# Performance work log

Measured on AMD Instinct MI355X. Metric: run time of the kernel, lower is better.

The kernel has to match this reference:

```python
import jax, jax.numpy as jnp
import numpy as np

N_EMB = 1024
HEAD_SIZE = 64
BLOCK_SIZE = 2048
B, T = 8, 2048


def setup_inputs() -> dict:
    key = jax.random.key(0)
    kx, kq, kk, kv = jax.random.split(key, 4)
    scale = 1.0 / (N_EMB ** 0.5)
    x = jax.random.normal(kx, (B, T, N_EMB), dtype=jnp.float32)
    Wq = jax.random.uniform(kq, (N_EMB, HEAD_SIZE), dtype=jnp.float32) * scale
    Wk = jax.random.uniform(kk, (N_EMB, HEAD_SIZE), dtype=jnp.float32) * scale
    Wv = jax.random.uniform(kv, (N_EMB, HEAD_SIZE), dtype=jnp.float32) * scale
    return {"x": x, "Wq": Wq, "Wk": Wk, "Wv": Wv}


def reference(x, Wq, Wk, Wv):
    # Faithful to Head.__call__ with is_training=False.
    # NOTE: original code applies NO 1/sqrt(head_size) scaling to the scores.
    Bt, Tt, _ = x.shape
    q = x @ Wq                      # (B, T, H)
    k = x @ Wk                      # (B, T, H)
    v = x @ Wv                      # (B, T, H)
    wei = jnp.einsum('bth,bsh->bts', q, k)  # (B, T, T)
    causal = jnp.tril(jnp.ones((Tt, Tt), dtype=bool))
    wei = jnp.where(causal, wei, -jnp.inf)
    wei = jax.nn.softmax(wei, axis=-1)
    out = jnp.einsum('bts,bsh->bth', wei, v)  # (B, T, H)
    return out
```

## Files before the change

### kernel.cpp

```cpp
#include <hip/hip_runtime.h>
#include <hip/hip_bf16.h>

#define BB 8
#define TT 2048
#define EE 1024
#define HH 64

typedef __attribute__((ext_vector_type(8))) short short8;
typedef __attribute__((ext_vector_type(4))) float f32x4;

__device__ inline f32x4 mfma_16x16x32(short8 a, short8 b, f32x4 c) {
  return __builtin_amdgcn_mfma_f32_16x16x32_bf16(a, b, c, 0, 0, 0);
}

__device__ inline void gload_lds16(const __hip_bfloat16* g, __hip_bfloat16* l) {
  __builtin_amdgcn_global_load_lds((const __attribute__((address_space(1))) void*)g,
                                   (__attribute__((address_space(3))) void*)l,
                                   16, 0, 0);
}

__device__ inline short f2bf(float f) {
  __hip_bfloat16 h = __float2bfloat16(f);
  return *reinterpret_cast<short*>(&h);
}
__device__ inline float bf2f(short s) {
  __hip_bfloat16 h = *reinterpret_cast<__hip_bfloat16*>(&s);
  return __bfloat162float(h);
}

#define WAIT_LGKM0() __builtin_amdgcn_s_waitcnt(0xC07F)

__global__ void prep_w(const float* __restrict__ Wq, const float* __restrict__ Wk,
                       const float* __restrict__ Wv,
                       __hip_bfloat16* __restrict__ Wthi,
                       __hip_bfloat16* __restrict__ Wtlo) {
  const int n = blockIdx.x;
  const int m = n >> 6;
  const int h = n & 63;
  const float* W = (m == 0) ? Wq : (m == 1) ? Wk : Wv;
  const int e0 = threadIdx.x * 4;
#pragma unroll
  for (int j = 0; j < 4; ++j) {
    const float w = W[(e0 + j) * 64 + h];
    const __hip_bfloat16 hi = __float2bfloat16(w);
    Wthi[n * 1024 + e0 + j] = hi;
    Wtlo[n * 1024 + e0 + j] = __float2bfloat16(w - __bfloat162float(hi));
  }
}

__global__ __launch_bounds__(256) void qkv_gemm(
    const float* __restrict__ x,
    const __hip_bfloat16* __restrict__ Wthi, const __hip_bfloat16* __restrict__ Wtlo,
    __hip_bfloat16* __restrict__ qhi, __hip_bfloat16* __restrict__ qlo,
    __hip_bfloat16* __restrict__ khi, __hip_bfloat16* __restrict__ klo,
    __hip_bfloat16* __restrict__ vT) {
  __shared__ __hip_bfloat16 Ahi[2][64 * 72];
  __shared__ __hip_bfloat16 Alo[2][64 * 72];
  __shared__ __hip_bfloat16 Bhi[2][192 * 64];
  __shared__ __hip_bfloat16 Blo[2][128 * 64];

  const int tid  = threadIdx.x;
  const int wave = tid >> 6;
  const int lane = tid & 63;
  const int row0 = blockIdx.x * 64;

  const int lr = tid >> 2;
  const int le = (tid & 3) * 16;
  const float* xrow = x + (row0 + lr) * 1024 + le;

  f32x4 acc[12];
#pragma unroll
  for (int j = 0; j < 12; ++j) acc[j] = f32x4{0.f, 0.f, 0.f, 0.f};

  const int l15 = lane & 15, l4 = lane >> 4;

  auto issue_B = [&](int c, int buf) {
    const int g = (lane & 7) ^ ((lane >> 3) & 7);
#pragma unroll
    for (int s = 0; s < 6; ++s) {
      const int qq = wave * 6 + s;
      const int n  = qq * 8 + (lane >> 3);
      gload_lds16(Wthi + n * 1024 + c * 64 + g * 8, &Bhi[buf][qq * 512]);
      if (qq < 16)
        gload_lds16(Wtlo + n * 1024 + c * 64 + g * 8, &Blo[buf][qq * 512]);
    }
  };
  auto write_A = [&](int buf, const f32x4* xr) {
    short8 h0, h1, l0, l1;
    const float* xf = (const float*)xr;
#pragma unroll
    for (int j = 0; j < 8; ++j) {
      const float v = xf[j];
      const short h = f2bf(v);
      h0[j] = h;
      l0[j] = f2bf(v - bf2f(h));
    }
#pragma unroll
    for (int j = 0; j < 8; ++j) {
      const float v = xf[8 + j];
      const short h = f2bf(v);
      h1[j] = h;
      l1[j] = f2bf(v - bf2f(h));
    }
    *(short8*)&Ahi[buf][lr * 72 + le]     = h0;
    *(short8*)&Ahi[buf][lr * 72 + le + 8] = h1;
    *(short8*)&Alo[buf][lr * 72 + le]     = l0;
    *(short8*)&Alo[buf][lr * 72 + le + 8] = l1;
  };
  auto compute = [&](int buf) {
    const int tr = wave * 16 + l15;
    short8 ah0 = *(const short8*)&Ahi[buf][tr * 72 + l4 * 8];
    short8 ah1 = *(const short8*)&Ahi[buf][tr * 72 + 32 + l4 * 8];
    short8 al0 = *(const short8*)&Alo[buf][tr * 72 + l4 * 8];
    short8 al1 = *(const short8*)&Alo[buf][tr * 72 + 32 + l4 * 8];
#pragma unroll
    for (int j = 0; j < 12; ++j) {
      const int n  = j * 16 + l15;
      const int o0 = ((l4)     ^ (n & 7)) * 8;
      const int o1 = ((4 + l4) ^ (n & 7)) * 8;
      short8 bh0 = *(const short8*)&Bhi[buf][n * 64 + o0];
      short8 bh1 = *(const short8*)&Bhi[buf][n * 64 + o1];
      acc[j] = mfma_16x16x32(ah0, bh0, acc[j]);
      acc[j] = mfma_16x16x32(ah1, bh1, acc[j]);
      if (j < 8) {
        short8 bl0 = *(const short8*)&Blo[buf][n * 64 + o0];
        short8 bl1 = *(const short8*)&Blo[buf][n * 64 + o1];
        acc[j] = mfma_16x16x32(ah0, bl0, acc[j]);
        acc[j] = mfma_16x16x32(ah1, bl1, acc[j]);
        acc[j] = mfma_16x16x32(al0, bh0, acc[j]);
        acc[j] = mfma_16x16x32(al1, bh1, acc[j]);
      }
    }
  };

  f32x4 xr[4], xn[4];
  {
    const f32x4* p = (const f32x4*)xrow;
    xr[0] = p[0]; xr[1] = p[1]; xr[2] = p[2]; xr[3] = p[3];
  }
  issue_B(0, 0);
  __builtin_amdgcn_s_waitcnt(0);
  write_A(0, xr);
  __syncthreads();

  for (int c = 0; c < 16; ++c) {
    const int p = c & 1;
    if (c < 15) {
      const f32x4* pp = (const f32x4*)(xrow + (c + 1) * 64);
      xn[0] = pp[0]; xn[1] = pp[1]; xn[2] = pp[2]; xn[3] = pp[3];
      issue_B(c + 1, p ^ 1);
    }
    compute(p);
    if (c < 15) {
      __builtin_amdgcn_s_waitcnt(0);
      write_A(p ^ 1, xn);
    }
    __syncthreads();
  }

  const int strip = wave * 16;
#pragma unroll
  for (int j = 0; j < 12; ++j) {
    const int n  = j * 16 + l15;
    const int mm = n >> 6;
    const int h  = n & 63;
#pragma unroll
    for (int r = 0; r < 4; ++r) {
      const int trow = row0 + strip + l4 * 4 + r;
      const float val = acc[j][r];
      const __hip_bfloat16 hi = __float2bfloat16(val);
      const __hip_bfloat16 lo = __float2bfloat16(val - __bfloat162float(hi));
      if (mm == 0) {
        qhi[trow * 64 + h] = hi;
        qlo[trow * 64 + h] = lo;
      } else if (mm == 1) {
        khi[trow * 64 + h] = hi;
        klo[trow * 64 + h] = lo;
      } else {
        const int bb = trow >> 11, tl = trow & 2047;
        vT[(bb * 64 + h) * 2048 + tl] = hi;
      }
    }
  }
}

__global__ __launch_bounds__(256, 2) void attn(
    const __hip_bfloat16* __restrict__ qhi, const __hip_bfloat16* __restrict__ qlo,
    const __hip_bfloat16* __restrict__ khi, const __hip_bfloat16* __restrict__ klo,
    const __hip_bfloat16* __restrict__ vT, float* __restrict__ out) {
  __shared__ __hip_bfloat16 Psm[4][2][16 * 72];
  __shared__ float Osm[4][32][65];
  __shared__ float Msm[4][32];
  __shared__ float Lsm[4][32];

  const int tid  = threadIdx.x;
  const int wave = tid >> 6;
  const int lane = tid & 63;
  const int l15 = lane & 15, l4 = lane >> 4;

  const int b  = blockIdx.x & 7;
  const int ss = 63 - (blockIdx.x >> 3);
  const int t0 = ss * 32;
  const int ntiles = (ss >> 1) + 1;

  short8 qh0[2], qh1[2], ql0[2], ql1[2];
#pragma unroll
  for (int m = 0; m < 2; ++m) {
    const __hip_bfloat16* qph = qhi + (b * 2048 + t0 + m * 16 + l15) * 64;
    const __hip_bfloat16* qpl = qlo + (b * 2048 + t0 + m * 16 + l15) * 64;
    qh0[m] = *(const short8*)(qph + l4 * 8);
    qh1[m] = *(const short8*)(qph + 32 + l4 * 8);
    ql0[m] = *(const short8*)(qpl + l4 * 8);
    ql1[m] = *(const short8*)(qpl + 32 + l4 * 8);
  }

  f32x4 acc[2][4];
#pragma unroll
  for (int m = 0; m < 2; ++m)
#pragma unroll
    for (int j = 0; j < 4; ++j) acc[m][j] = f32x4{0.f, 0.f, 0.f, 0.f};
  float m_[2][4], l_[2][4];
#pragma unroll
  for (int m = 0; m < 2; ++m)
#pragma unroll
    for (int r = 0; r < 4; ++r) { m_[m][r] = -1e30f; l_[m][r] = 0.f; }

  const __hip_bfloat16* kbase_h = khi + (size_t)b * 2048 * 64;
  const __hip_bfloat16* kbase_l = klo + (size_t)b * 2048 * 64;
  const __hip_bfloat16* vbase   = vT + (size_t)b * 64 * 2048;

  for (int kt = wave; kt < ntiles; kt += 4) {
    const int k0 = kt << 6;
    const bool diag = (kt == ntiles - 1);

    short8 kh0[4], kh1[4], kl0[4], kl1[4];
#pragma unroll
    for (int j = 0; j < 4; ++j) {
      const __hip_bfloat16* kph = kbase_h + (k0 + j * 16 + l15) * 64;
      const __hip_bfloat16* kpl = kbase_l + (k0 + j * 16 + l15) * 64;
      kh0[j] = *(const short8*)(kph + l4 * 8);
      kh1[j] = *(const short8*)(kph + 32 + l4 * 8);
      kl0[j] = *(const short8*)(kpl + l4 * 8);
      kl1[j] = *(const short8*)(kpl + 32 + l4 * 8);
    }

#pragma unroll
    for (int m = 0; m < 2; ++m) {
      const int rowbase = t0 + m * 16;
      f32x4 s_[4];
#pragma unroll
      for (int j = 0; j < 4; ++j) {
        if (diag && (k0 + j * 16) > (rowbase + 15)) {
          s_[j] = f32x4{-1e30f, -1e30f, -1e30f, -1e30f};
          continue;
        }
        f32x4 z = f32x4{0.f, 0.f, 0.f, 0.f};
        z = mfma_16x16x32(qh0[m], kh0[j], z);
        z = mfma_16x16x32(qh1[m], kh1[j], z);
        z = mfma_16x16x32(qh0[m], kl0[j], z);
        z = mfma_16x16x32(qh1[m], kl1[j], z);
        z = mfma_16x16x32(ql0[m], kh0[j], z);
        z = mfma_16x16x32(ql1[m], kh1[j], z);
        s_[j] = z;
      }
      if (diag) {
#pragma unroll
        for (int j = 0; j < 4; ++j) {
          const int key = k0 + j * 16 + l15;
#pragma unroll
          for (int r = 0; r < 4; ++r) {
            const int row = rowbase + l4 * 4 + r;
            if (key > row) s_[j][r] = -1e30f;
          }
        }
      }

      float mx[4], rs[4], al[4];
#pragma unroll
      for (int r = 0; r < 4; ++r)
        mx[r] = fmaxf(fmaxf(s_[0][r], s_[1][r]), fmaxf(s_[2][r], s_[3][r]));
      for (int off = 1; off < 16; off <<= 1) {
#pragma unroll
        for (int r = 0; r < 4; ++r) mx[r] = fmaxf(mx[r], __shfl_xor(mx[r], off));
      }
#pragma unroll
      for (int r = 0; r < 4; ++r) {
        const float mn = fmaxf(m_[m][r], mx[r]);
        al[r] = __expf(m_[m][r] - mn);
        m_[m][r] = mn;
        rs[r] = 0.f;
      }
#pragma unroll
      for (int j = 0; j < 4; ++j) {
#pragma unroll
        for (int r = 0; r < 4; ++r) {
          const float pv = __expf(s_[j][r] - m_[m][r]);
          s_[j][r] = pv;
          rs[r] += pv;
        }
      }
      for (int off = 1; off < 16; off <<= 1) {
#pragma unroll
        for (int r = 0; r < 4; ++r) rs[r] += __shfl_xor(rs[r], off);
      }
#pragma unroll
      for (int r = 0; r < 4; ++r) l_[m][r] = l_[m][r] * al[r] + rs[r];
#pragma unroll
      for (int j = 0; j < 4; ++j)
#pragma unroll
        for (int r = 0; r < 4; ++r) acc[m][j][r] *= al[r];

#pragma unroll
      for (int j = 0; j < 4; ++j)
#pragma unroll
        for (int r = 0; r < 4; ++r)
          Psm[wave][m][(l4 * 4 + r) * 72 + j * 16 + l15] =
              __float2bfloat16(s_[j][r]);
    }

    short8 vf0[4], vf1[4];
#pragma unroll
    for (int j = 0; j < 4; ++j) {
      const __hip_bfloat16* vp = vbase + (j * 16 + l15) * 2048 + k0;
      vf0[j] = *(const short8*)(vp + l4 * 8);
      vf1[j] = *(const short8*)(vp + 32 + l4 * 8);
    }

    WAIT_LGKM0();

#pragma unroll
    for (int m = 0; m < 2; ++m) {
      short8 pf0 = *(const short8*)&Psm[wave][m][l15 * 72 + l4 * 8];
      short8 pf1 = *(const short8*)&Psm[wave][m][l15 * 72 + 32 + l4 * 8];
#pragma unroll
      for (int j = 0; j < 4; ++j) {
        acc[m][j] = mfma_16x16x32(pf0, vf0[j], acc[m][j]);
        acc[m][j] = mfma_16x16x32(pf1, vf1[j], acc[m][j]);
      }
    }
  }

#pragma unroll
  for (int m = 0; m < 2; ++m) {
#pragma unroll
    for (int j = 0; j < 4; ++j)
#pragma unroll
      for (int r = 0; r < 4; ++r)
        Osm[wave][m * 16 + l4 * 4 + r][j * 16 + l15] = acc[m][j][r];
    if (l15 == 0) {
#pragma unroll
      for (int r = 0; r < 4; ++r) {
        Msm[wave][m * 16 + l4 * 4 + r] = m_[m][r];
        Lsm[wave][m * 16 + l4 * 4 + r] = l_[m][r];
      }
    }
  }
  __syncthreads();

#pragma unroll
  for (int rr = 0; rr < 8; ++rr) {
    const int row = wave * 8 + rr;
    float M = fmaxf(fmaxf(Msm[0][row], Msm[1][row]),
                    fmaxf(Msm[2][row], Msm[3][row]));
    float L = 0.f, O = 0.f;
#pragma unroll
    for (int w2 = 0; w2 < 4; ++w2) {
      const float a = __expf(Msm[w2][row] - M);
      L += a * Lsm[w2][row];
      O += a * Osm[w2][row][lane];
    }
    out[(b * 2048 + t0 + row) * 64 + lane] = O / L;
  }
}

extern "C" void kernel_launch(void* const* d_in, const int* in_sizes, int n_in,
                              void* d_out, int out_size, void* d_ws, size_t ws_size,
                              hipStream_t stream) {
  const float* x  = (const float*)d_in[0];
  const float* Wq = (const float*)d_in[1];
  const float* Wk = (const float*)d_in[2];
  const float* Wv = (const float*)d_in[3];
  float* out = (float*)d_out;

  char* ws = (char*)d_ws;
  __hip_bfloat16* Wthi = (__hip_bfloat16*)ws;
  __hip_bfloat16* Wtlo = (__hip_bfloat16*)(ws + 393216);
  __hip_bfloat16* qhi  = (__hip_bfloat16*)(ws + 786432);
  __hip_bfloat16* qlo  = (__hip_bfloat16*)(ws + 786432 + 1 * 2097152);
  __hip_bfloat16* khi  = (__hip_bfloat16*)(ws + 786432 + 2 * 2097152);
  __hip_bfloat16* klo  = (__hip_bfloat16*)(ws + 786432 + 3 * 2097152);
  __hip_bfloat16* vT   = (__hip_bfloat16*)(ws + 786432 + 4 * 2097152);

  prep_w<<<192, 256, 0, stream>>>(Wq, Wk, Wv, Wthi, Wtlo);
  qkv_gemm<<<256, 256, 0, stream>>>(x, Wthi, Wtlo, qhi, qlo, khi, klo, vT);
  attn<<<512, 256, 0, stream>>>(qhi, qlo, khi, klo, vT, out);
}
```

Measured before the change: 159.6 us.

## Replace online softmax max tracking with precomputed per-row Cauchy-Schwarz bias

Adds two small prep kernels that compute each batch's max key squared norm and, per query row, a fixed softmax offset equal to max(q·k_self, |q|·max|k| - 85). The attention kernel then subtracts this fixed offset instead of tracking a running max, which removes the max shuffles, the rescale exps, the accumulator rescaling and the cross-wave max merge. It also prefetches the next tile's K-hi fragments and issues V loads earlier so they overlap the score MFMAs. The fixed offset risks overflow or underflow of exp when the real scores sit far from the bound. It also adds two extra kernel launches.

```diff
diff --git a/kernel.cpp b/kernel.cpp
--- a/kernel.cpp
+++ b/kernel.cpp
@@ -184,13 +184,68 @@
   }
 }
 
+__global__ __launch_bounds__(256) void prep_maxk(
+    const __hip_bfloat16* __restrict__ khi, const __hip_bfloat16* __restrict__ klo,
+    float* __restrict__ maxK2) {
+  __shared__ float red[256];
+  const int b = blockIdx.x;
+  float mx = 0.f;
+  for (int t = threadIdx.x; t < 2048; t += 256) {
+    const short8* vh = (const short8*)(khi + (b * 2048 + t) * 64);
+    const short8* vl = (const short8*)(klo + (b * 2048 + t) * 64);
+    float s = 0.f;
+#pragma unroll
+    for (int g = 0; g < 8; ++g) {
+      short8 a = vh[g], c = vl[g];
+#pragma unroll
+      for (int i = 0; i < 8; ++i) {
+        const float v = bf2f(a[i]) + bf2f(c[i]);
+        s += v * v;
+      }
+    }
+    mx = fmaxf(mx, s);
+  }
+  red[threadIdx.x] = mx;
+  __syncthreads();
+  for (int o = 128; o > 0; o >>= 1) {
+    if (threadIdx.x < o) red[threadIdx.x] = fmaxf(red[threadIdx.x], red[threadIdx.x + o]);
+    __syncthreads();
+  }
+  if (threadIdx.x == 0) maxK2[b] = red[0];
+}
+
+__global__ __launch_bounds__(256) void prep_bias(
+    const __hip_bfloat16* __restrict__ qhi, const __hip_bfloat16* __restrict__ qlo,
+    const __hip_bfloat16* __restrict__ khi, const __hip_bfloat16* __restrict__ klo,
+    const float* __restrict__ maxK2, float* __restrict__ bias) {
+  const int t = blockIdx.x * 256 + threadIdx.x;
+  const int b = t >> 11;
+  const short8* qh = (const short8*)(qhi + t * 64);
+  const short8* ql = (const short8*)(qlo + t * 64);
+  const short8* kh = (const short8*)(khi + t * 64);
+  const short8* kl = (const short8*)(klo + t * 64);
+  float dot = 0.f, q2 = 0.f;
+#pragma unroll
+  for (int g = 0; g < 8; ++g) {
+    short8 a = qh[g], c = ql[g], d = kh[g], e = kl[g];
+#pragma unroll
+    for (int i = 0; i < 8; ++i) {
+      const float qv = bf2f(a[i]) + bf2f(c[i]);
+      const float kv = bf2f(d[i]) + bf2f(e[i]);
+      dot += qv * kv;
+      q2  += qv * qv;
+    }
+  }
+  bias[t] = fmaxf(dot, sqrtf(q2 * maxK2[b]) - 85.f);
+}
+
 __global__ __launch_bounds__(256, 2) void attn(
     const __hip_bfloat16* __restrict__ qhi, const __hip_bfloat16* __restrict__ qlo,
     const __hip_bfloat16* __restrict__ khi, const __hip_bfloat16* __restrict__ klo,
-    const __hip_bfloat16* __restrict__ vT, float* __restrict__ out) {
+    const __hip_bfloat16* __restrict__ vT, const float* __restrict__ bias,
+    float* __restrict__ out) {
   __shared__ __hip_bfloat16 Psm[4][2][16 * 72];
   __shared__ float Osm[4][32][65];
-  __shared__ float Msm[4][32];
   __shared__ float Lsm[4][32];
 
   const int tid  = threadIdx.x;
@@ -214,34 +269,68 @@
     ql1[m] = *(const short8*)(qpl + 32 + l4 * 8);
   }
 
+  float bs_[2][4];
+#pragma unroll
+  for (int m = 0; m < 2; ++m)
+#pragma unroll
+    for (int r = 0; r < 4; ++r)
+      bs_[m][r] = bias[b * 2048 + t0 + m * 16 + l4 * 4 + r];
+
   f32x4 acc[2][4];
 #pragma unroll
   for (int m = 0; m < 2; ++m)
 #pragma unroll
     for (int j = 0; j < 4; ++j) acc[m][j] = f32x4{0.f, 0.f, 0.f, 0.f};
-  float m_[2][4], l_[2][4];
+  float l_[2][4];
 #pragma unroll
   for (int m = 0; m < 2; ++m)
 #pragma unroll
-    for (int r = 0; r < 4; ++r) { m_[m][r] = -1e30f; l_[m][r] = 0.f; }
+    for (int r = 0; r < 4; ++r) l_[m][r] = 0.f;
 
   const __hip_bfloat16* kbase_h = khi + (size_t)b * 2048 * 64;
   const __hip_bfloat16* kbase_l = klo + (size_t)b * 2048 * 64;
   const __hip_bfloat16* vbase   = vT + (size_t)b * 64 * 2048;
 
-  for (int kt = wave; kt < ntiles; kt += 4) {
+  short8 ch0[4], ch1[4];
+  int kt = wave;
+  if (kt < ntiles) {
+    const int k0 = kt << 6;
+#pragma unroll
+    for (int j = 0; j < 4; ++j) {
+      const __hip_bfloat16* kph = kbase_h + (k0 + j * 16 + l15) * 64;
+      ch0[j] = *(const short8*)(kph + l4 * 8);
+      ch1[j] = *(const short8*)(kph + 32 + l4 * 8);
+    }
+  }
+
+  for (; kt < ntiles; kt += 4) {
     const int k0 = kt << 6;
     const bool diag = (kt == ntiles - 1);
 
-    short8 kh0[4], kh1[4], kl0[4], kl1[4];
+    short8 cl0[4], cl1[4];
 #pragma unroll
     for (int j = 0; j < 4; ++j) {
-      const __hip_bfloat16* kph = kbase_h + (k0 + j * 16 + l15) * 64;
       const __hip_bfloat16* kpl = kbase_l + (k0 + j * 16 + l15) * 64;
-      kh0[j] = *(const short8*)(kph + l4 * 8);
-      kh1[j] = *(const short8*)(kph + 32 + l4 * 8);
-      kl0[j] = *(const short8*)(kpl + l4 * 8);
-      kl1[j] = *(const short8*)(kpl + 32 + l4 * 8);
+      cl0[j] = *(const short8*)(kpl + l4 * 8);
+      cl1[j] = *(const short8*)(kpl + 32 + l4 * 8);
+    }
+    short8 nh0[4], nh1[4];
+    {
+      const int ktn = (kt + 4 < ntiles) ? kt + 4 : kt;
+      const int k0n = ktn << 6;
+#pragma unroll
+      for (int j = 0; j < 4; ++j) {
+        const __hip_bfloat16* kph = kbase_h + (k0n + j * 16 + l15) * 64;
+        nh0[j] = *(const short8*)(kph + l4 * 8);
+        nh1[j] = *(const short8*)(kph + 32 + l4 * 8);
+      }
+    }
+    short8 vf0[4], vf1[4];
+#pragma unroll
+    for (int j = 0; j < 4; ++j) {
+      const __hip_bfloat16* vp = vbase + (j * 16 + l15) * 2048 + k0;
+      vf0[j] = *(const short8*)(vp + l4 * 8);
+      vf1[j] = *(const short8*)(vp + 32 + l4 * 8);
     }
 
 #pragma unroll
@@ -255,12 +344,12 @@
           continue;
         }
         f32x4 z = f32x4{0.f, 0.f, 0.f, 0.f};
-        z = mfma_16x16x32(qh0[m], kh0[j], z);
-        z = mfma_16x16x32(qh1[m], kh1[j], z);
-        z = mfma_16x16x32(qh0[m], kl0[j], z);
-        z = mfma_16x16x32(qh1[m], kl1[j], z);
-        z = mfma_16x16x32(ql0[m], kh0[j], z);
-        z = mfma_16x16x32(ql1[m], kh1[j], z);
+        z = mfma_16x16x32(qh0[m], ch0[j], z);
+        z = mfma_16x16x32(qh1[m], ch1[j], z);
+        z = mfma_16x16x32(ql0[m], ch0[j], z);
+        z = mfma_16x16x32(ql1[m], ch1[j], z);
+        z = mfma_16x16x32(qh0[m], cl0[j], z);
+        z = mfma_16x16x32(qh1[m], cl1[j], z);
         s_[j] = z;
       }
       if (diag) {
@@ -275,40 +364,15 @@
         }
       }
 
-      float mx[4], rs[4], al[4];
-#pragma unroll
-      for (int r = 0; r < 4; ++r)
-        mx[r] = fmaxf(fmaxf(s_[0][r], s_[1][r]), fmaxf(s_[2][r], s_[3][r]));
-      for (int off = 1; off < 16; off <<= 1) {
-#pragma unroll
-        for (int r = 0; r < 4; ++r) mx[r] = fmaxf(mx[r], __shfl_xor(mx[r], off));
-      }
-#pragma unroll
-      for (int r = 0; r < 4; ++r) {
-        const float mn = fmaxf(m_[m][r], mx[r]);
-        al[r] = __expf(m_[m][r] - mn);
-        m_[m][r] = mn;
-        rs[r] = 0.f;
-      }
 #pragma unroll
       for (int j = 0; j < 4; ++j) {
 #pragma unroll
         for (int r = 0; r < 4; ++r) {
-          const float pv = __expf(s_[j][r] - m_[m][r]);
+          const float pv = __expf(s_[j][r] - bs_[m][r]);
           s_[j][r] = pv;
-          rs[r] += pv;
+          l_[m][r] += pv;
         }
       }
-      for (int off = 1; off < 16; off <<= 1) {
-#pragma unroll
-        for (int r = 0; r < 4; ++r) rs[r] += __shfl_xor(rs[r], off);
-      }
-#pragma unroll
-      for (int r = 0; r < 4; ++r) l_[m][r] = l_[m][r] * al[r] + rs[r];
-#pragma unroll
-      for (int j = 0; j < 4; ++j)
-#pragma unroll
-        for (int r = 0; r < 4; ++r) acc[m][j][r] *= al[r];
 
 #pragma unroll
       for (int j = 0; j < 4; ++j)
@@ -318,14 +382,6 @@
               __float2bfloat16(s_[j][r]);
     }
 
-    short8 vf0[4], vf1[4];
-#pragma unroll
-    for (int j = 0; j < 4; ++j) {
-      const __hip_bfloat16* vp = vbase + (j * 16 + l15) * 2048 + k0;
-      vf0[j] = *(const short8*)(vp + l4 * 8);
-      vf1[j] = *(const short8*)(vp + 32 + l4 * 8);
-    }
-
     WAIT_LGKM0();
 
 #pragma unroll
@@ -338,7 +394,17 @@
         acc[m][j] = mfma_16x16x32(pf1, vf1[j], acc[m][j]);
       }
     }
-  }
+
+#pragma unroll
+    for (int j = 0; j < 4; ++j) { ch0[j] = nh0[j]; ch1[j] = nh1[j]; }
+  }
+
+#pragma unroll
+  for (int m = 0; m < 2; ++m)
+    for (int off = 1; off < 16; off <<= 1) {
+#pragma unroll
+      for (int r = 0; r < 4; ++r) l_[m][r] += __shfl_xor(l_[m][r], off);
+    }
 
 #pragma unroll
   for (int m = 0; m < 2; ++m) {
@@ -349,10 +415,8 @@
         Osm[wave][m * 16 + l4 * 4 + r][j * 16 + l15] = acc[m][j][r];
     if (l15 == 0) {
 #pragma unroll
-      for (int r = 0; r < 4; ++r) {
-        Msm[wave][m * 16 + l4 * 4 + r] = m_[m][r];
+      for (int r = 0; r < 4; ++r)
         Lsm[wave][m * 16 + l4 * 4 + r] = l_[m][r];
-      }
     }
   }
   __syncthreads();
@@ -360,15 +424,9 @@
 #pragma unroll
   for (int rr = 0; rr < 8; ++rr) {
     const int row = wave * 8 + rr;
-    float M = fmaxf(fmaxf(Msm[0][row], Msm[1][row]),
-                    fmaxf(Msm[2][row], Msm[3][row]));
-    float L = 0.f, O = 0.f;
-#pragma unroll
-    for (int w2 = 0; w2 < 4; ++w2) {
-      const float a = __expf(Msm[w2][row] - M);
-      L += a * Lsm[w2][row];
-      O += a * Osm[w2][row][lane];
-    }
+    float L = Lsm[0][row] + Lsm[1][row] + Lsm[2][row] + Lsm[3][row];
+    float O = Osm[0][row][lane] + Osm[1][row][lane] +
+              Osm[2][row][lane] + Osm[3][row][lane];
     out[(b * 2048 + t0 + row) * 64 + lane] = O / L;
   }
 }
@@ -390,8 +448,13 @@
   __hip_bfloat16* khi  = (__hip_bfloat16*)(ws + 786432 + 2 * 2097152);
   __hip_bfloat16* klo  = (__hip_bfloat16*)(ws + 786432 + 3 * 2097152);
   __hip_bfloat16* vT   = (__hip_bfloat16*)(ws + 786432 + 4 * 2097152);
+  char* p = ws + 786432 + 5 * 2097152;
+  float* maxK2 = (float*)p;
+  float* biasb = (float*)(p + 256);
 
   prep_w<<<192, 256, 0, stream>>>(Wq, Wk, Wv, Wthi, Wtlo);
   qkv_gemm<<<256, 256, 0, stream>>>(x, Wthi, Wtlo, qhi, qlo, khi, klo, vT);
-  attn<<<512, 256, 0, stream>>>(qhi, qlo, khi, klo, vT, out);
-}
+  prep_maxk<<<8, 256, 0, stream>>>(khi, klo, maxK2);
+  prep_bias<<<64, 256, 0, stream>>>(qhi, qlo, khi, klo, maxK2, biasb);
+  attn<<<512, 256, 0, stream>>>(qhi, qlo, khi, klo, vT, biasb, out);
+}
```

Measured after the change: 214.1 us. +34.1%, slower.
